# Performance work log

Measured on AMD Instinct MI355X. Metric: run time of the kernel, lower is better.

The kernel has to match this reference:

```python
import math
import jax, jax.numpy as jnp
import numpy as np

L, H, W_SIZE, EPS = 4, 4, 64, 1e-5


def _sinusoidal_pe(T, D):
    pos = np.arange(T, dtype=np.float32)[:, None]
    div = np.exp(np.arange(0, D, 2, dtype=np.float32) * -(math.log(10000.0) / D))
    pe = np.zeros((T, D), dtype=np.float32)
    pe[:, 0::2] = np.sin(pos * div)
    pe[:, 1::2] = np.cos(pos * div)
    return jnp.asarray(pe)


def _layernorm(x, g, b):
    mu = jnp.mean(x, axis=-1, keepdims=True)
    var = jnp.mean(jnp.square(x - mu), axis=-1, keepdims=True)
    return (x - mu) * jax.lax.rsqrt(var + EPS) * g + b


def setup_inputs() -> dict:
    key = jax.random.key(0)
    B, T, D, F = 4, 2048, 256, 1024
    ks = jax.random.split(key, 8)
    s = 0.02
    return {
        "tokens": jax.random.normal(ks[0], (B, T, D), jnp.float32),
        "Wqkv": jax.random.normal(ks[1], (L, 3 * D, D), jnp.float32) * s,
        "bqkv": jnp.zeros((L, 3 * D), jnp.float32),
        "Wo": jax.random.normal(ks[2], (L, D, D), jnp.float32) * s,
        "bo": jnp.zeros((L, D), jnp.float32),
        "W1": jax.random.normal(ks[3], (L, F, D), jnp.float32) * s,
        "b1": jnp.zeros((L, F), jnp.float32),
        "W2": jax.random.normal(ks[4], (L, D, F), jnp.float32) * s,
        "b2": jnp.zeros((L, D), jnp.float32),
        "ln1_g": jnp.ones((L, D), jnp.float32),
        "ln1_b": jnp.zeros((L, D), jnp.float32),
        "ln2_g": jnp.ones((L, D), jnp.float32),
        "ln2_b": jnp.zeros((L, D), jnp.float32),
        "lnf_g": jnp.ones((D,), jnp.float32),
        "lnf_b": jnp.zeros((D,), jnp.float32),
    }


def reference(tokens, Wqkv, bqkv, Wo, bo, W1, b1, W2, b2,
              ln1_g, ln1_b, ln2_g, ln2_b, lnf_g, lnf_b):
    B, T, D = tokens.shape
    hd = D // H
    x = tokens + _sinusoidal_pe(T, D)[None]  # (B,T,D)

    # sliding-window causal mask: i attends to max(0, i-W+1)..i
    idx = jnp.arange(T)
    i, j = idx[:, None], idx[None, :]
    allowed = (j <= i) & (j >= i - W_SIZE + 1)
    bias = jnp.where(allowed, 0.0, -1e9).astype(jnp.float32)  # (T,T)

    def step(x, p):
        Wqkv, bqkv, Wo, bo, W1, b1, W2, b2, g1, be1, g2, be2 = p
        x2 = _layernorm(x, g1, be1)
        qkv = x2 @ Wqkv.T + bqkv                      # (B,T,3D)
        q, k, v = jnp.split(qkv, 3, axis=-1)
        q = q.reshape(B, T, H, hd)
        k = k.reshape(B, T, H, hd)
        v = v.reshape(B, T, H, hd)
        scores = jnp.einsum("bthd,bshd->bhts", q, k) / math.sqrt(hd)
        attn = jax.nn.softmax(scores + bias, axis=-1)
        o = jnp.einsum("bhts,bshd->bthd", attn, v).reshape(B, T, D)
        x = x + o @ Wo.T + bo
        x3 = _layernorm(x, g2, be2)
        h = jax.nn.gelu(x3 @ W1.T + b1, approximate=False)
        x = x + h @ W2.T + b2
        return x, None

    x, _ = jax.lax.scan(step, x, (Wqkv, bqkv, Wo, bo, W1, b1, W2, b2,
                                  ln1_g, ln1_b, ln2_g, ln2_b))
    return _layernorm(x, lnf_g, lnf_b)
```

## Files before the change

kernel.cpp:

```cpp
#include <hip/hip_runtime.h>
#include <hip/hip_bf16.h>
#include <math.h>

#define BB 4
#define TT 2048
#define DD 256
#define FF 1024
#define NL 4

typedef __bf16 bf16x8 __attribute__((ext_vector_type(8)));
typedef float f32x4 __attribute__((ext_vector_type(4)));

__device__ __forceinline__ void stage16(const __hip_bfloat16* gp, __hip_bfloat16* lp) {
  __builtin_amdgcn_global_load_lds(
      (const __attribute__((address_space(1))) unsigned int*)gp,
      (__attribute__((address_space(3))) unsigned int*)lp, 16, 0, 0);
}

__device__ __forceinline__ float gelu_f(float v) {
  float x = fabsf(v) * 0.70710678118654752f;
  float t = 1.0f / fmaf(0.3275911f, x, 1.0f);
  float p = t * fmaf(t, fmaf(t, fmaf(t, fmaf(t, 1.061405429f, -1.453152027f),
                                     1.421413741f), -0.284496736f), 0.254829592f);
  float erfv = copysignf(1.0f - p * __expf(-x * x), v);
  return 0.5f * v * (1.0f + erfv);
}

__global__ __launch_bounds__(256) void prologue_kernel(
    const float4* __restrict__ wq, const float4* __restrict__ wo,
    const float4* __restrict__ w1, const float4* __restrict__ w2,
    ushort4* __restrict__ dst,
    const float* __restrict__ tokens, const float* __restrict__ g,
    const float* __restrict__ b, float* __restrict__ x,
    __hip_bfloat16* __restrict__ sb) {
  if (blockIdx.x < 3072) {
    int gi = blockIdx.x * 256 + threadIdx.x;
    const float4* src;
    int off;
    if (gi < 196608)      { src = wq; off = gi; }
    else if (gi < 262144) { src = wo; off = gi - 196608; }
    else if (gi < 524288) { src = w1; off = gi - 262144; }
    else                  { src = w2; off = gi - 524288; }
    float4 v = src[off];
    ushort4 o;
    o.x = __hip_bfloat16_raw(__float2bfloat16(v.x)).x;
    o.y = __hip_bfloat16_raw(__float2bfloat16(v.y)).x;
    o.z = __hip_bfloat16_raw(__float2bfloat16(v.z)).x;
    o.w = __hip_bfloat16_raw(__float2bfloat16(v.w)).x;
    dst[gi] = o;
    return;
  }
  int row = (blockIdx.x - 3072) * 4 + (threadIdx.x >> 6);
  int lane = threadIdx.x & 63;
  int t = row & (TT - 1);
  const float* xr = tokens + (size_t)row * DD;
  float v[4];
  float s = 0.f;
#pragma unroll
  for (int i = 0; i < 4; ++i) {
    int d = lane + 64 * i;
    int i2 = d & ~1;
    float freq = expf((float)i2 * -(9.210340371976184f / 256.f));
    float ang = (float)t * freq;
    float pe = (d & 1) ? cosf(ang) : sinf(ang);
    v[i] = xr[d] + pe;
    s += v[i];
  }
#pragma unroll
  for (int off = 32; off; off >>= 1) s += __shfl_xor(s, off, 64);
  float mu = s * (1.f / DD);
  float vs = 0.f;
#pragma unroll
  for (int i = 0; i < 4; ++i) { float dd = v[i] - mu; vs = fmaf(dd, dd, vs); }
#pragma unroll
  for (int off = 32; off; off >>= 1) vs += __shfl_xor(vs, off, 64);
  float rr = rsqrtf(vs * (1.f / DD) + 1e-5f);
#pragma unroll
  for (int i = 0; i < 4; ++i) {
    int d = lane + 64 * i;
    x[(size_t)row * DD + d] = v[i];
    sb[(size_t)row * DD + d] = __float2bfloat16((v[i] - mu) * rr * g[d] + b[d]);
  }
}

template <int MW, int NW, int BK, int KTOT, int ACT, int OUTF>
__global__ __launch_bounds__(256) void mgemm_kernel(
    const __hip_bfloat16* __restrict__ A, const __hip_bfloat16* __restrict__ B,
    const float* __restrict__ bias, void* __restrict__ Cout,
    int M, int N) {
  constexpr int BM = 32 * MW, BN = 32 * NW, ROWS = BM + BN;
  constexpr int NCH = BK / 32;
  constexpr int CHB = ROWS * 32;
  constexpr int RG = ROWS / 16;
  constexpr int NST = NCH * RG;
  __shared__ __align__(16) __hip_bfloat16 sm[NCH * CHB];
  const int tid = threadIdx.x;
  const int wave = tid >> 6, lane = tid & 63;
  const int m0 = blockIdx.y * BM, n0 = blockIdx.x * BN;
  const int wm = (wave >> 1) * (16 * MW), wn = (wave & 1) * (16 * NW);
  const int quad = lane >> 4, lr = lane & 15;
  const int srow = lane >> 2, scol = (lane & 3) * 8;

  f32x4 acc[MW][NW] = {};

  for (int kt = 0; kt < KTOT; kt += BK) {
    __syncthreads();
#pragma unroll
    for (int i = 0; i < NST / 4; ++i) {
      int inst = i * 4 + wave;
      int c = inst / RG, grp = inst - c * RG;
      int r = grp * 16 + srow;
      const __hip_bfloat16* gp =
          (r < BM) ? (A + (size_t)(m0 + r) * KTOT + kt + c * 32 + scol)
                   : (B + (size_t)(n0 + (r - BM)) * KTOT + kt + c * 32 + scol);
      stage16(gp, sm + c * CHB + grp * 512);
    }
    __syncthreads();
#pragma unroll
    for (int c = 0; c < NCH; ++c) {
      bf16x8 af[MW], bfr[NW];
#pragma unroll
      for (int mi = 0; mi < MW; ++mi)
        af[mi] = *(const bf16x8*)(sm + c * CHB + (wm + mi * 16 + lr) * 32 + quad * 8);
#pragma unroll
      for (int ni = 0; ni < NW; ++ni)
        bfr[ni] = *(const bf16x8*)(sm + c * CHB + (BM + wn + ni * 16 + lr) * 32 + quad * 8);
#pragma unroll
      for (int mi = 0; mi < MW; ++mi)
#pragma unroll
        for (int ni = 0; ni < NW; ++ni)
          acc[mi][ni] = __builtin_amdgcn_mfma_f32_16x16x32_bf16(
              af[mi], bfr[ni], acc[mi][ni], 0, 0, 0);
    }
  }

#pragma unroll
  for (int mi = 0; mi < MW; ++mi) {
#pragma unroll
    for (int ni = 0; ni < NW; ++ni) {
      int col = n0 + wn + ni * 16 + lr;
      float bv = bias[col];
#pragma unroll
      for (int r = 0; r < 4; ++r) {
        int row = m0 + wm + mi * 16 + quad * 4 + r;
        float v = acc[mi][ni][r] + bv;
        if (ACT == 1) v = gelu_f(v);
        if (OUTF) ((float*)Cout)[(size_t)row * N + col] = v;
        else ((__hip_bfloat16*)Cout)[(size_t)row * N + col] = __float2bfloat16(v);
      }
    }
  }
}

template <int KTOT>
__global__ __launch_bounds__(256) void mgemm_ln_kernel(
    const __hip_bfloat16* __restrict__ A, const __hip_bfloat16* __restrict__ B,
    const float* __restrict__ bias, const float* __restrict__ res,
    const float* __restrict__ g, const float* __restrict__ bb,
    float* __restrict__ xout, __hip_bfloat16* __restrict__ yout) {
  constexpr int BM = 32, ROWS = BM + 256;
  constexpr int BK = 64, NCH = BK / 32;
  constexpr int CHB = ROWS * 32;
  constexpr int RG = ROWS / 16;
  constexpr int NST = NCH * RG;
  __shared__ __align__(16) __hip_bfloat16 sm[NCH * CHB];
  __shared__ float red1[4][BM], red2[4][BM];
  const int tid = threadIdx.x;
  const int wave = tid >> 6, lane = tid & 63;
  const int quad = lane >> 4, lr = lane & 15;
  const int m0 = blockIdx.x * BM;
  const int srow = lane >> 2, scol = (lane & 3) * 8;

  f32x4 acc[2][4] = {};

  for (int kt = 0; kt < KTOT; kt += BK) {
    __syncthreads();
#pragma unroll
    for (int i = 0; i < NST / 4; ++i) {
      int inst = i * 4 + wave;
      int c = inst / RG, grp = inst - c * RG;
      int r = grp * 16 + srow;
      const __hip_bfloat16* gp =
          (r < BM) ? (A + (size_t)(m0 + r) * KTOT + kt + c * 32 + scol)
                   : (B + (size_t)(r - BM) * KTOT + kt + c * 32 + scol);
      stage16(gp, sm + c * CHB + grp * 512);
    }
    __syncthreads();
#pragma unroll
    for (int c = 0; c < NCH; ++c) {
      bf16x8 af[2], bfr[4];
#pragma unroll
      for (int mi = 0; mi < 2; ++mi)
        af[mi] = *(const bf16x8*)(sm + c * CHB + (mi * 16 + lr) * 32 + quad * 8);
#pragma unroll
      for (int ni = 0; ni < 4; ++ni)
        bfr[ni] = *(const bf16x8*)(sm + c * CHB + (BM + wave * 64 + ni * 16 + lr) * 32 + quad * 8);
#pragma unroll
      for (int mi = 0; mi < 2; ++mi)
#pragma unroll
        for (int ni = 0; ni < 4; ++ni)
          acc[mi][ni] = __builtin_amdgcn_mfma_f32_16x16x32_bf16(
              af[mi], bfr[ni], acc[mi][ni], 0, 0, 0);
    }
  }

  float v[2][4][4];
  float s1[2][4] = {}, s2[2][4] = {};
#pragma unroll
  for (int mi = 0; mi < 2; ++mi)
#pragma unroll
    for (int ni = 0; ni < 4; ++ni) {
      int col = wave * 64 + ni * 16 + lr;
      float bv = bias[col];
#pragma unroll
      for (int r = 0; r < 4; ++r) {
        int row = m0 + mi * 16 + quad * 4 + r;
        float val = acc[mi][ni][r] + bv + res[(size_t)row * DD + col];
        v[mi][ni][r] = val;
        s1[mi][r] += val;
        s2[mi][r] = fmaf(val, val, s2[mi][r]);
      }
    }
#pragma unroll
  for (int mi = 0; mi < 2; ++mi)
#pragma unroll
    for (int r = 0; r < 4; ++r) {
#pragma unroll
      for (int off = 8; off; off >>= 1) {
        s1[mi][r] += __shfl_xor(s1[mi][r], off, 64);
        s2[mi][r] += __shfl_xor(s2[mi][r], off, 64);
      }
    }
  if (lr == 0) {
#pragma unroll
    for (int mi = 0; mi < 2; ++mi)
#pragma unroll
      for (int r = 0; r < 4; ++r) {
        red1[wave][mi * 16 + quad * 4 + r] = s1[mi][r];
        red2[wave][mi * 16 + quad * 4 + r] = s2[mi][r];
      }
  }
  __syncthreads();
#pragma unroll
  for (int mi = 0; mi < 2; ++mi)
#pragma unroll
    for (int r = 0; r < 4; ++r) {
      int rl = mi * 16 + quad * 4 + r;
      float ssum = red1[0][rl] + red1[1][rl] + red1[2][rl] + red1[3][rl];
      float qsum = red2[0][rl] + red2[1][rl] + red2[2][rl] + red2[3][rl];
      float mu = ssum * (1.f / DD);
      float var = qsum * (1.f / DD) - mu * mu;
      float rr = rsqrtf(var + 1e-5f);
      int row = m0 + rl;
#pragma unroll
      for (int ni = 0; ni < 4; ++ni) {
        int col = wave * 64 + ni * 16 + lr;
        float y = (v[mi][ni][r] - mu) * rr * g[col] + bb[col];
        yout[(size_t)row * DD + col] = __float2bfloat16(y);
        xout[(size_t)row * DD + col] = v[mi][ni][r];
      }
    }
}

template <int FIN>
__global__ __launch_bounds__(256) void rln_kernel(
    const float* __restrict__ go, const float* __restrict__ xin,
    const float* __restrict__ g, const float* __restrict__ b,
    float* __restrict__ xout, __hip_bfloat16* __restrict__ sbout,
    float* __restrict__ out) {
  int row = blockIdx.x * 4 + (threadIdx.x >> 6);
  int lane = threadIdx.x & 63;
  const float* gr = go + (size_t)row * DD;
  const float* xr = xin + (size_t)row * DD;
  float v[4];
  float s = 0.f;
#pragma unroll
  for (int i = 0; i < 4; ++i) {
    int d = lane + 64 * i;
    v[i] = gr[d] + xr[d];
    s += v[i];
  }
#pragma unroll
  for (int off = 32; off; off >>= 1) s += __shfl_xor(s, off, 64);
  float mu = s * (1.f / DD);
  float vs = 0.f;
#pragma unroll
  for (int i = 0; i < 4; ++i) { float dd = v[i] - mu; vs = fmaf(dd, dd, vs); }
#pragma unroll
  for (int off = 32; off; off >>= 1) vs += __shfl_xor(vs, off, 64);
  float rr = rsqrtf(vs * (1.f / DD) + 1e-5f);
#pragma unroll
  for (int i = 0; i < 4; ++i) {
    int d = lane + 64 * i;
    float y = (v[i] - mu) * rr * g[d] + b[d];
    if (FIN) {
      out[(size_t)row * DD + d] = y;
    } else {
      xout[(size_t)row * DD + d] = v[i];
      sbout[(size_t)row * DD + d] = __float2bfloat16(y);
    }
  }
}

__global__ __launch_bounds__(256) void attn_kernel(const __hip_bfloat16* __restrict__ qkv,
                                                   __hip_bfloat16* __restrict__ o) {
  __shared__ __align__(16) __hip_bfloat16 KsPs[128 * 72];
  __shared__ __align__(16) __hip_bfloat16 Vt[64 * 136];
  const int bh = blockIdx.y;
  const int b = bh >> 2, h = bh & 3;
  const int t0 = blockIdx.x * 64;
  const int sbase = t0 - 63;
  const int tid = threadIdx.x;

  const __hip_bfloat16* kb = qkv + (size_t)(b * TT) * 768 + 256 + h * 64;
  const __hip_bfloat16* vb = kb + 256;
  union U8 { uint4 u; __hip_bfloat16 hx[8]; };
#pragma unroll
  for (int it = 0; it < 4; ++it) {
    int f = tid + it * 256;
    int si = f >> 3;
    int c8 = f & 7;
    int s = sbase + si;
    U8 kr, vr;
    kr.u = make_uint4(0, 0, 0, 0); vr.u = make_uint4(0, 0, 0, 0);
    if (s >= 0 && s < TT) {
      kr.u = *(const uint4*)&kb[(size_t)s * 768 + 8 * c8];
      vr.u = *(const uint4*)&vb[(size_t)s * 768 + 8 * c8];
    }
    *(uint4*)&KsPs[si * 72 + c8 * 8] = kr.u;
    int pc = (si >> 3) ^ c8;
#pragma unroll
    for (int j = 0; j < 8; ++j) Vt[(c8 * 8 + j) * 136 + pc * 8 + (si & 7)] = vr.hx[j];
  }
  __syncthreads();

  const int wave = tid >> 6, lane = tid & 63;
  const int quad = lane >> 4, lr = lane & 15;

  const __hip_bfloat16* qrow = qkv + (size_t)(b * TT + t0 + wave * 16 + lr) * 768 + h * 64;
  bf16x8 qa0 = *(const bf16x8*)(qrow + quad * 8);
  bf16x8 qa1 = *(const bf16x8*)(qrow + 32 + quad * 8);
  f32x4 sc[8];
#pragma unroll
  for (int c = 0; c < 8; ++c) {
    f32x4 a = {};
    bf16x8 kf0 = *(const bf16x8*)&KsPs[(c * 16 + lr) * 72 + quad * 8];
    a = __builtin_amdgcn_mfma_f32_16x16x32_bf16(qa0, kf0, a, 0, 0, 0);
    bf16x8 kf1 = *(const bf16x8*)&KsPs[(c * 16 + lr) * 72 + 32 + quad * 8];
    a = __builtin_amdgcn_mfma_f32_16x16x32_bf16(qa1, kf1, a, 0, 0, 0);
    sc[c] = a;
  }
  __syncthreads();

#pragma unroll
  for (int reg = 0; reg < 4; ++reg) {
    int dt = wave * 16 + quad * 4 + reg;
    float pv[8];
    float mx = -1e30f;
#pragma unroll
    for (int c = 0; c < 8; ++c) {
      int si = c * 16 + lr;
      float v = sc[c][reg] * 0.125f;
      bool ok = (si >= dt) && (si <= dt + 63) && (sbase + si >= 0);
      v = ok ? v : -1e30f;
      pv[c] = v;
      mx = fmaxf(mx, v);
    }
#pragma unroll
    for (int off = 8; off; off >>= 1) mx = fmaxf(mx, __shfl_xor(mx, off, 64));
    float l = 0.f;
#pragma unroll
    for (int c = 0; c < 8; ++c) { float e = __expf(pv[c] - mx); pv[c] = e; l += e; }
#pragma unroll
    for (int off = 8; off; off >>= 1) l += __shfl_xor(l, off, 64);
    float rinv = 1.f / l;
#pragma unroll
    for (int c = 0; c < 8; ++c)
      KsPs[(wave * 16 + quad * 4 + reg) * 136 + c * 16 + lr] = __float2bfloat16(pv[c] * rinv);
  }

  __hip_bfloat16* obase = o + (size_t)(b * TT) * DD + h * 64;
#pragma unroll
  for (int ct = 0; ct < 4; ++ct) {
    f32x4 acc = {};
#pragma unroll
    for (int kk = 0; kk < 4; ++kk) {
      bf16x8 pa = *(const bf16x8*)&KsPs[(wave * 16 + lr) * 136 + kk * 32 + quad * 8];
      int dd = ct * 16 + lr;
      bf16x8 vf = *(const bf16x8*)&Vt[dd * 136 + (((kk * 4 + quad) ^ (dd >> 3)) * 8)];
      acc = __builtin_amdgcn_mfma_f32_16x16x32_bf16(pa, vf, acc, 0, 0, 0);
    }
#pragma unroll
    for (int reg = 0; reg < 4; ++reg) {
      int t = t0 + wave * 16 + quad * 4 + reg;
      obase[(size_t)t * DD + ct * 16 + lr] = __float2bfloat16(acc[reg]);
    }
  }
}

extern "C" void kernel_launch(void* const* d_in, const int* in_sizes, int n_in,
                              void* d_out, int out_size, void* d_ws, size_t ws_size,
                              hipStream_t stream) {
  const float* tokens = (const float*)d_in[0];
  const float* Wqkv = (const float*)d_in[1];
  const float* bqkv = (const float*)d_in[2];
  const float* Wo   = (const float*)d_in[3];
  const float* bo   = (const float*)d_in[4];
  const float* W1   = (const float*)d_in[5];
  const float* b1   = (const float*)d_in[6];
  const float* W2   = (const float*)d_in[7];
  const float* b2   = (const float*)d_in[8];
  const float* ln1g = (const float*)d_in[9];
  const float* ln1b = (const float*)d_in[10];
  const float* ln2g = (const float*)d_in[11];
  const float* ln2b = (const float*)d_in[12];
  const float* lnfg = (const float*)d_in[13];
  const float* lnfb = (const float*)d_in[14];
  float* out = (float*)d_out;

  const int M = BB * TT;
  const int ND = M * DD;

  float* x = (float*)d_ws;
  __hip_bfloat16* sb  = (__hip_bfloat16*)(x + ND);
  __hip_bfloat16* big = sb + (size_t)M * DD;
  __hip_bfloat16* wqb = big + (size_t)M * FF;
  __hip_bfloat16* wob = wqb + (size_t)NL * 3 * DD * DD;
  __hip_bfloat16* w1b = wob + (size_t)NL * DD * DD;
  __hip_bfloat16* w2b = w1b + (size_t)NL * FF * DD;
  float* gbuf = (float*)(w2b + (size_t)NL * DD * FF);

  prologue_kernel<<<3072 + M / 4, 256, 0, stream>>>(
      (const float4*)Wqkv, (const float4*)Wo, (const float4*)W1,
      (const float4*)W2, (ushort4*)wqb, tokens, ln1g, ln1b, x, sb);

  mgemm_kernel<2, 4, 64, 256, 0, 0><<<dim3(6, 128), 256, 0, stream>>>(
      sb, wqb, bqkv, big, M, 768);

  for (int l = 0; l < NL; ++l) {
    attn_kernel<<<dim3(TT / 64, BB * 4), 256, 0, stream>>>(big, sb);
    mgemm_ln_kernel<256><<<M / 32, 256, 0, stream>>>(
        sb, wob + (size_t)l * DD * DD, bo + l * DD, x,
        ln2g + l * DD, ln2b + l * DD, x, sb);
    mgemm_kernel<2, 4, 64, 256, 1, 0><<<dim3(8, 128), 256, 0, stream>>>(
        sb, w1b + (size_t)l * FF * DD, b1 + l * FF, big, M, FF);
    mgemm_kernel<2, 2, 64, 1024, 0, 1><<<dim3(4, 128), 256, 0, stream>>>(
        big, w2b + (size_t)l * DD * FF, b2 + l * DD, gbuf, M, DD);
    if (l < NL - 1) {
      rln_kernel<0><<<M / 4, 256, 0, stream>>>(
          gbuf, x, ln1g + (l + 1) * DD, ln1b + (l + 1) * DD, x, sb, nullptr);
      mgemm_kernel<2, 4, 64, 256, 0, 0><<<dim3(6, 128), 256, 0, stream>>>(
          sb, wqb + (size_t)(l + 1) * 768 * DD, bqkv + (l + 1) * 768, big, M, 768);
    } else {
      rln_kernel<1><<<M / 4, 256, 0, stream>>>(
          gbuf, x, lnfg, lnfb, nullptr, nullptr, out);
    }
  }
}
```

Baseline: 361.1 us.

## Remap GEMM blocks per XCD, deepen K tile, store FFN2 output in bf16

The GEMM kernel now takes a 1D grid and maps block ids so that each of the 8 XCDs (blocks are assigned round-robin by bid&7) works on a contiguous band of M tiles, which improves per-XCD L2 reuse of A rows. BK is doubled from 64 to 128, halving the number of sync/stage rounds at the cost of more LDS per block and possibly lower occupancy. The FFN2 output buffer gbuf changes from fp32 to bf16 and rln_kernel reads bf16, cutting write and read traffic. That adds rounding error on the residual update.

Result: no change. 354.5 us (-1.8%).

```diff
diff --git a/kernel.cpp b/kernel.cpp
--- a/kernel.cpp
+++ b/kernel.cpp
@@ -10,8 +10,9 @@
 
 typedef __bf16 bf16x8 __attribute__((ext_vector_type(8)));
 typedef float f32x4 __attribute__((ext_vector_type(4)));
-
-__device__ __forceinline__ void stage16(const __hip_bfloat16* gp, __hip_bfloat16* lp) {
+typedef __hip_bfloat16 bf16;
+
+__device__ __forceinline__ void stage16(const bf16* gp, bf16* lp) {
   __builtin_amdgcn_global_load_lds(
       (const __attribute__((address_space(1))) unsigned int*)gp,
       (__attribute__((address_space(3))) unsigned int*)lp, 16, 0, 0);
@@ -32,7 +33,7 @@
     ushort4* __restrict__ dst,
     const float* __restrict__ tokens, const float* __restrict__ g,
     const float* __restrict__ b, float* __restrict__ x,
-    __hip_bfloat16* __restrict__ sb) {
+    bf16* __restrict__ sb) {
   if (blockIdx.x < 3072) {
     int gi = blockIdx.x * 256 + threadIdx.x;
     const float4* src;
@@ -59,8 +60,7 @@
 #pragma unroll
   for (int i = 0; i < 4; ++i) {
     int d = lane + 64 * i;
-    int i2 = d & ~1;
-    float freq = expf((float)i2 * -(9.210340371976184f / 256.f));
+    float freq = expf((float)(d & ~1) * -(9.210340371976184f / 256.f));
     float ang = (float)t * freq;
     float pe = (d & 1) ? cosf(ang) : sinf(ang);
     v[i] = xr[d] + pe;
@@ -85,18 +85,22 @@
 
 template <int MW, int NW, int BK, int KTOT, int ACT, int OUTF>
 __global__ __launch_bounds__(256) void mgemm_kernel(
-    const __hip_bfloat16* __restrict__ A, const __hip_bfloat16* __restrict__ B,
+    const bf16* __restrict__ A, const bf16* __restrict__ B,
     const float* __restrict__ bias, void* __restrict__ Cout,
-    int M, int N) {
+    int N, int nN, int nM) {
   constexpr int BM = 32 * MW, BN = 32 * NW, ROWS = BM + BN;
   constexpr int NCH = BK / 32;
   constexpr int CHB = ROWS * 32;
   constexpr int RG = ROWS / 16;
   constexpr int NST = NCH * RG;
-  __shared__ __align__(16) __hip_bfloat16 sm[NCH * CHB];
+  __shared__ __align__(16) bf16 sm[NCH * CHB];
   const int tid = threadIdx.x;
   const int wave = tid >> 6, lane = tid & 63;
-  const int m0 = blockIdx.y * BM, n0 = blockIdx.x * BN;
+  const int bid = blockIdx.x;
+  const int xcd = bid & 7, kk = bid >> 3;
+  const int mt = xcd * (nM >> 3) + kk / nN;
+  const int nt = kk - (kk / nN) * nN;
+  const int m0 = mt * BM, n0 = nt * BN;
   const int wm = (wave >> 1) * (16 * MW), wn = (wave & 1) * (16 * NW);
   const int quad = lane >> 4, lr = lane & 15;
   const int srow = lane >> 2, scol = (lane & 3) * 8;
@@ -110,7 +114,7 @@
       int inst = i * 4 + wave;
       int c = inst / RG, grp = inst - c * RG;
       int r = grp * 16 + srow;
-      const __hip_bfloat16* gp =
+      const bf16* gp =
           (r < BM) ? (A + (size_t)(m0 + r) * KTOT + kt + c * 32 + scol)
                    : (B + (size_t)(n0 + (r - BM)) * KTOT + kt + c * 32 + scol);
       stage16(gp, sm + c * CHB + grp * 512);
@@ -135,7 +139,7 @@
   }
 
 #pragma unroll
-  for (int mi = 0; mi < MW; ++mi) {
+  for (int mi = 0; mi < MW; ++mi)
 #pragma unroll
     for (int ni = 0; ni < NW; ++ni) {
       int col = n0 + wn + ni * 16 + lr;
@@ -146,24 +150,23 @@
         float v = acc[mi][ni][r] + bv;
         if (ACT == 1) v = gelu_f(v);
         if (OUTF) ((float*)Cout)[(size_t)row * N + col] = v;
-        else ((__hip_bfloat16*)Cout)[(size_t)row * N + col] = __float2bfloat16(v);
+        else ((bf16*)Cout)[(size_t)row * N + col] = __float2bfloat16(v);
       }
     }
-  }
 }
 
 template <int KTOT>
 __global__ __launch_bounds__(256) void mgemm_ln_kernel(
-    const __hip_bfloat16* __restrict__ A, const __hip_bfloat16* __restrict__ B,
+    const bf16* __restrict__ A, const bf16* __restrict__ B,
     const float* __restrict__ bias, const float* __restrict__ res,
     const float* __restrict__ g, const float* __restrict__ bb,
-    float* __restrict__ xout, __hip_bfloat16* __restrict__ yout) {
+    float* __restrict__ xout, bf16* __restrict__ yout) {
   constexpr int BM = 32, ROWS = BM + 256;
   constexpr int BK = 64, NCH = BK / 32;
   constexpr int CHB = ROWS * 32;
   constexpr int RG = ROWS / 16;
   constexpr int NST = NCH * RG;
-  __shared__ __align__(16) __hip_bfloat16 sm[NCH * CHB];
+  __shared__ __align__(16) bf16 sm[NCH * CHB];
   __shared__ float red1[4][BM], red2[4][BM];
   const int tid = threadIdx.x;
   const int wave = tid >> 6, lane = tid & 63;
@@ -180,7 +183,7 @@
       int inst = i * 4 + wave;
       int c = inst / RG, grp = inst - c * RG;
       int r = grp * 16 + srow;
-      const __hip_bfloat16* gp =
+      const bf16* gp =
           (r < BM) ? (A + (size_t)(m0 + r) * KTOT + kt + c * 32 + scol)
                    : (B + (size_t)(r - BM) * KTOT + kt + c * 32 + scol);
       stage16(gp, sm + c * CHB + grp * 512);
@@ -264,20 +267,20 @@
 
 template <int FIN>
 __global__ __launch_bounds__(256) void rln_kernel(
-    const float* __restrict__ go, const float* __restrict__ xin,
+    const bf16* __restrict__ go, const float* __restrict__ xin,
     const float* __restrict__ g, const float* __restrict__ b,
-    float* __restrict__ xout, __hip_bfloat16* __restrict__ sbout,
+    float* __restrict__ xout, bf16* __restrict__ sbout,
     float* __restrict__ out) {
   int row = blockIdx.x * 4 + (threadIdx.x >> 6);
   int lane = threadIdx.x & 63;
-  const float* gr = go + (size_t)row * DD;
+  const bf16* gr = go + (size_t)row * DD;
   const float* xr = xin + (size_t)row * DD;
   float v[4];
   float s = 0.f;
 #pragma unroll
   for (int i = 0; i < 4; ++i) {
     int d = lane + 64 * i;
-    v[i] = gr[d] + xr[d];
+    v[i] = __bfloat162float(gr[d]) + xr[d];
     s += v[i];
   }
 #pragma unroll
@@ -302,19 +305,19 @@
   }
 }
 
-__global__ __launch_bounds__(256) void attn_kernel(const __hip_bfloat16* __restrict__ qkv,
-                                                   __hip_bfloat16* __restrict__ o) {
-  __shared__ __align__(16) __hip_bfloat16 KsPs[128 * 72];
-  __shared__ __align__(16) __hip_bfloat16 Vt[64 * 136];
+__global__ __launch_bounds__(256) void attn_kernel(const bf16* __restrict__ qkv,
+                                                   bf16* __restrict__ o) {
+  __shared__ __align__(16) bf16 KsPs[128 * 72];
+  __shared__ __align__(16) bf16 Vt[64 * 136];
   const int bh = blockIdx.y;
   const int b = bh >> 2, h = bh & 3;
   const int t0 = blockIdx.x * 64;
   const int sbase = t0 - 63;
   const int tid = threadIdx.x;
 
-  const __hip_bfloat16* kb = qkv + (size_t)(b * TT) * 768 + 256 + h * 64;
-  const __hip_bfloat16* vb = kb + 256;
-  union U8 { uint4 u; __hip_bfloat16 hx[8]; };
+  const bf16* kb = qkv + (size_t)(b * TT) * 768 + 256 + h * 64;
+  const bf16* vb = kb + 256;
+  union U8 { uint4 u; bf16 hx[8]; };
 #pragma unroll
   for (int it = 0; it < 4; ++it) {
     int f = tid + it * 256;
@@ -337,7 +340,7 @@
   const int wave = tid >> 6, lane = tid & 63;
   const int quad = lane >> 4, lr = lane & 15;
 
-  const __hip_bfloat16* qrow = qkv + (size_t)(b * TT + t0 + wave * 16 + lr) * 768 + h * 64;
+  const bf16* qrow = qkv + (size_t)(b * TT + t0 + wave * 16 + lr) * 768 + h * 64;
   bf16x8 qa0 = *(const bf16x8*)(qrow + quad * 8);
   bf16x8 qa1 = *(const bf16x8*)(qrow + 32 + quad * 8);
   f32x4 sc[8];
@@ -379,7 +382,7 @@
       KsPs[(wave * 16 + quad * 4 + reg) * 136 + c * 16 + lr] = __float2bfloat16(pv[c] * rinv);
   }
 
-  __hip_bfloat16* obase = o + (size_t)(b * TT) * DD + h * 64;
+  bf16* obase = o + (size_t)(b * TT) * DD + h * 64;
 #pragma unroll
   for (int ct = 0; ct < 4; ++ct) {
     f32x4 acc = {};
@@ -422,35 +425,35 @@
   const int ND = M * DD;
 
   float* x = (float*)d_ws;
-  __hip_bfloat16* sb  = (__hip_bfloat16*)(x + ND);
-  __hip_bfloat16* big = sb + (size_t)M * DD;
-  __hip_bfloat16* wqb = big + (size_t)M * FF;
-  __hip_bfloat16* wob = wqb + (size_t)NL * 3 * DD * DD;
-  __hip_bfloat16* w1b = wob + (size_t)NL * DD * DD;
-  __hip_bfloat16* w2b = w1b + (size_t)NL * FF * DD;
-  float* gbuf = (float*)(w2b + (size_t)NL * DD * FF);
+  bf16* sb  = (bf16*)(x + ND);
+  bf16* big = sb + (size_t)M * DD;
+  bf16* wqb = big + (size_t)M * FF;
+  bf16* wob = wqb + (size_t)NL * 3 * DD * DD;
+  bf16* w1b = wob + (size_t)NL * DD * DD;
+  bf16* w2b = w1b + (size_t)NL * FF * DD;
+  bf16* gbuf = w2b + (size_t)NL * DD * FF;
 
   prologue_kernel<<<3072 + M / 4, 256, 0, stream>>>(
       (const float4*)Wqkv, (const float4*)Wo, (const float4*)W1,
       (const float4*)W2, (ushort4*)wqb, tokens, ln1g, ln1b, x, sb);
 
-  mgemm_kernel<2, 4, 64, 256, 0, 0><<<dim3(6, 128), 256, 0, stream>>>(
-      sb, wqb, bqkv, big, M, 768);
+  mgemm_kernel<2, 4, 128, 256, 0, 0><<<768, 256, 0, stream>>>(
+      sb, wqb, bqkv, big, 768, 6, 128);
 
   for (int l = 0; l < NL; ++l) {
     attn_kernel<<<dim3(TT / 64, BB * 4), 256, 0, stream>>>(big, sb);
     mgemm_ln_kernel<256><<<M / 32, 256, 0, stream>>>(
         sb, wob + (size_t)l * DD * DD, bo + l * DD, x,
         ln2g + l * DD, ln2b + l * DD, x, sb);
-    mgemm_kernel<2, 4, 64, 256, 1, 0><<<dim3(8, 128), 256, 0, stream>>>(
-        sb, w1b + (size_t)l * FF * DD, b1 + l * FF, big, M, FF);
-    mgemm_kernel<2, 2, 64, 1024, 0, 1><<<dim3(4, 128), 256, 0, stream>>>(
-        big, w2b + (size_t)l * DD * FF, b2 + l * DD, gbuf, M, DD);
+    mgemm_kernel<2, 4, 128, 256, 1, 0><<<1024, 256, 0, stream>>>(
+        sb, w1b + (size_t)l * FF * DD, b1 + l * FF, big, FF, 8, 128);
+    mgemm_kernel<2, 2, 128, 1024, 0, 0><<<512, 256, 0, stream>>>(
+        big, w2b + (size_t)l * DD * FF, b2 + l * DD, gbuf, DD, 4, 128);
     if (l < NL - 1) {
       rln_kernel<0><<<M / 4, 256, 0, stream>>>(
           gbuf, x, ln1g + (l + 1) * DD, ln1b + (l + 1) * DD, x, sb, nullptr);
-      mgemm_kernel<2, 4, 64, 256, 0, 0><<<dim3(6, 128), 256, 0, stream>>>(
-          sb, wqb + (size_t)(l + 1) * 768 * DD, bqkv + (l + 1) * 768, big, M, 768);
+      mgemm_kernel<2, 4, 128, 256, 0, 0><<<768, 256, 0, stream>>>(
+          sb, wqb + (size_t)(l + 1) * 768 * DD, bqkv + (l + 1) * 768, big, 768, 6, 128);
     } else {
       rln_kernel<1><<<M / 4, 256, 0, stream>>>(
           gbuf, x, lnfg, lnfb, nullptr, nullptr, out);
```
